# Optimization experiments

Measured on AMD Instinct MI355X. Metric: run time of the kernel, lower is better.

## Reference

```python
import jax, jax.numpy as jnp
import numpy as np

HEADS = 8
C_OUT = 256


def _gconv1x1(x, w, g):
    # x: (B, Cin, H, W); w: (Cout, Cin//g) -> grouped 1x1 conv, out (B, g, Cout//g, L)
    B, C, H, W = x.shape
    xr = x.reshape(B, g, C // g, H * W)
    wr = w.reshape(g, w.shape[0] // g, C // g)
    return jnp.einsum('god,bgdl->bgol', wr, xr)


def _sine_pe(d, L, dtype):
    # standard transformer sinusoidal PE laid out as (channels=d, positions=L)
    pos = jnp.arange(L, dtype=jnp.float32)
    i = jnp.arange(0, d, 2, dtype=jnp.float32)
    inv_freq = jnp.exp(-np.float32(np.log(10000.0)) * i / d)  # (d/2,)
    ang = inv_freq[:, None] * pos[None, :]                    # (d/2, L)
    pe = jnp.zeros((d, L), jnp.float32)
    pe = pe.at[0::2].set(jnp.sin(ang)).at[1::2].set(jnp.cos(ang))
    return pe.astype(dtype)


def setup_inputs() -> dict:
    key = jax.random.key(0)
    k1, k2, k3, k4 = jax.random.split(key, 4)
    B, Cin, H, W = 2, 256, 24, 24
    std = np.float32(np.sqrt(2.0 / C_OUT))  # kaiming_normal fan_out, relu gain
    x = jax.random.normal(k1, (B, Cin, H, W), jnp.float32)
    wq = jax.random.normal(k2, (C_OUT, Cin // HEADS), jnp.float32) * std
    wk = jax.random.normal(k3, (C_OUT, Cin // HEADS), jnp.float32) * std
    wv = jax.random.normal(k4, (C_OUT, Cin // HEADS), jnp.float32) * std
    return {"x": x, "wq": wq, "wk": wk, "wv": wv}


def reference(x, wq, wk, wv):
    B, Cin, H, W = x.shape
    g = HEADS
    d = C_OUT // g
    L = H * W
    q = _gconv1x1(x, wq, g)  # (B, g, d, L)
    k = _gconv1x1(x, wk, g)
    v = _gconv1x1(x, wv, g)
    # sinusoidal positional encoding added to keys over flattened spatial dim
    pe = _sine_pe(C_OUT, L, x.dtype)
    k = (k.reshape(B, C_OUT, L) + pe[None]).reshape(B, g, d, L)
    # NOTE: original torch code flattens batch AND heads into the attention dim
    qf = q.transpose(0, 1, 3, 2).reshape(-1, d)   # (N, d), N = B*g*L
    kf = k.transpose(2, 0, 1, 3).reshape(d, -1)   # (d, N)
    vf = v.transpose(0, 1, 3, 2).reshape(-1, d)   # (N, d)
    scale = np.float32(np.sqrt(g / C_OUT))        # = 1/sqrt(d)
    att = jax.nn.softmax(qf @ kf * scale, axis=-1)  # (N, N)
    out = att @ vf                                  # (N, d)
    out = out.reshape(B, g, L, d).transpose(0, 1, 3, 2).reshape(B, C_OUT, H, W)
    return out
```

## Files before the change

kernel.cpp:

```cpp
#include <hip/hip_runtime.h>
#include <hip/hip_bf16.h>


#define LSP   576
#define NROW  9216
#define DH    32
#define NW    8
#define KPW   (NROW / NW)
#define BN    32
#define NTILE (KPW / BN)
#define PSTR  40
#define QB    36
#define SZ    ((size_t)NROW * DH)
#define SZP   (SZ + 2048)

typedef __attribute__((ext_vector_type(8))) short bh8;
typedef __attribute__((ext_vector_type(4))) float f4;

static __device__ __forceinline__ float bf2f(unsigned short u) {
    union { unsigned int i; float f; } w; w.i = (unsigned int)u << 16; return w.f;
}
static __device__ __forceinline__ unsigned short f2bf(float x) {
    union { float f; unsigned int i; } w; w.f = x;
    unsigned int u = w.i;
    return (unsigned short)((u + 0x7fffu + ((u >> 16) & 1u)) >> 16);
}
static __device__ __forceinline__ unsigned int pkbf(float a, float b) {
    union { __hip_bfloat162 h2; unsigned int u; } w;
    w.h2 = __float22bfloat162_rn(make_float2(a, b));
    return w.u;
}

#define MFMA(a, b, c) __builtin_amdgcn_mfma_f32_16x16x32_bf16(a, b, c, 0, 0, 0)

__global__ __launch_bounds__(256) void sa_proj_kernel(
    const float* __restrict__ x,
    const float* __restrict__ wq, const float* __restrict__ wk, const float* __restrict__ wv,
    unsigned short* __restrict__ Qhi, unsigned short* __restrict__ Qlo,
    unsigned short* __restrict__ Khi, unsigned short* __restrict__ Vt)
{
    __shared__ __align__(16) float xs[32 * 40];
    __shared__ float vt[32 * 37];
    __shared__ float wqs[32 * 33], wks[32 * 33], wvs[32 * 33];
    const int t = threadIdx.x;
    const int bg = blockIdx.x >> 4;
    const int part = blockIdx.x & 15;
    const int g = bg & 7;
    const int l0 = part * 36;

    const float* xp = x + (size_t)bg * 32 * LSP + l0;
    for (int i = t; i < 32 * 9; i += 256) {
        int d = i / 9, seg = i % 9;
        *(float4*)(xs + d * 40 + seg * 4) = *(const float4*)(xp + d * LSP + seg * 4);
    }
    for (int i = t; i < 1024; i += 256) {
        int o = i >> 5, d = i & 31;
        wqs[o * 33 + d] = wq[(g * 32 + o) * 32 + d];
        wks[o * 33 + d] = wk[(g * 32 + o) * 32 + d];
        wvs[o * 33 + d] = wv[(g * 32 + o) * 32 + d];
    }
    __syncthreads();

    const float scale = 0.17677669529663687f;
    for (int idx = t; idx < 32 * 36; idx += 256) {
        const int o = idx & 31;
        const int lloc = idx >> 5;
        const int l = l0 + lloc;
        float aq = 0.f, ak = 0.f, av = 0.f;
        #pragma unroll
        for (int d = 0; d < 32; d++) {
            const float xv = xs[d * 40 + lloc];
            aq = fmaf(wqs[o * 33 + d], xv, aq);
            ak = fmaf(wks[o * 33 + d], xv, ak);
            av = fmaf(wvs[o * 33 + d], xv, av);
        }
        aq *= scale;
        const int c = g * 32 + o;
        const float i2 = (float)(c & ~1);
        const float inv = __expf(-0.035977892078031968f * i2);
        float sv, cv;
        __sincosf(inv * (float)l, &sv, &cv);
        ak += (c & 1) ? cv : sv;

        const size_t row = (size_t)bg * LSP + l;
        const unsigned short h = f2bf(aq);
        Qhi[row * 32 + o] = h;
        Qlo[row * 32 + o] = f2bf(aq - bf2f(h));
        Khi[row * 32 + o] = f2bf(ak);
        vt[o * 37 + lloc] = av;
    }
    __syncthreads();

    for (int idx = t; idx < 32 * 36; idx += 256) {
        const int d = idx / 36;
        const int cc = idx - d * 36;
        const int n = bg * LSP + l0 + cc;
        const int k = n & 31;
        const int cperm = (k < 16) ? ((k >> 2) * 8 + (k & 3))
                                   : (((k - 16) >> 2) * 8 + ((k - 16) & 3) + 4);
        Vt[(size_t)(n >> 5) * 1024 + d * 32 + cperm] = f2bf(vt[d * 37 + cc]);
    }
}

__global__ __launch_bounds__(512, 2) void sa_attn_kernel(
    const unsigned short* __restrict__ Qhi, const unsigned short* __restrict__ Qlo,
    const unsigned short* __restrict__ Khi, const unsigned short* __restrict__ Vt,
    float* __restrict__ out)
{
    __shared__ __align__(16) unsigned short shm[NW * 2 * 48 * PSTR];
    const int t = threadIdx.x;
    const int wave = t >> 6, lane = t & 63;
    const int quad = lane >> 4, l16 = lane & 15;
    const int n0 = blockIdx.x * QB;

    unsigned short* psA = shm + wave * 2 * 48 * PSTR;
    unsigned short* psB = psA + 48 * PSTR;

    const bh8 qh0 = *(const bh8*)(Qhi + (size_t)(n0 + l16) * DH + quad * 8);
    const bh8 ql0 = *(const bh8*)(Qlo + (size_t)(n0 + l16) * DH + quad * 8);
    const bh8 qh1 = *(const bh8*)(Qhi + (size_t)(n0 + 16 + l16) * DH + quad * 8);
    const bh8 ql1 = *(const bh8*)(Qlo + (size_t)(n0 + 16 + l16) * DH + quad * 8);
    const bh8 qh2 = *(const bh8*)(Qhi + (size_t)(n0 + 32 + l16) * DH + quad * 8);
    const bh8 ql2 = *(const bh8*)(Qlo + (size_t)(n0 + 32 + l16) * DH + quad * 8);

    const short oneb = (short)0x3F80;
    const bh8 ones = {oneb, oneb, oneb, oneb, oneb, oneb, oneb, oneb};

    f4 o00 = {0.f,0.f,0.f,0.f}, o01 = {0.f,0.f,0.f,0.f};
    f4 o10 = {0.f,0.f,0.f,0.f}, o11 = {0.f,0.f,0.f,0.f};
    f4 o20 = {0.f,0.f,0.f,0.f}, o21 = {0.f,0.f,0.f,0.f};
    f4 lo0 = {0.f,0.f,0.f,0.f}, lo1 = {0.f,0.f,0.f,0.f}, lo2 = {0.f,0.f,0.f,0.f};
    const f4 zf = {0.f,0.f,0.f,0.f};

    const int kbase = wave * KPW;
    const int tile0 = kbase >> 5;

    bh8 kf0 = *(const bh8*)(Khi + (size_t)(kbase + l16) * DH + quad * 8);
    bh8 kf1 = *(const bh8*)(Khi + (size_t)(kbase + 16 + l16) * DH + quad * 8);
    bh8 vf0 = *(const bh8*)(Vt + (size_t)tile0 * 1024 + l16 * 32 + quad * 8);
    bh8 vf1 = *(const bh8*)(Vt + (size_t)tile0 * 1024 + (16 + l16) * 32 + quad * 8);
    bh8 pv0 = vf0, pv1 = vf1;

    for (int tile = 0; tile < NTILE; ++tile) {
        f4 s00 = MFMA(kf0, ql0, zf); s00 = MFMA(kf0, qh0, s00);
        f4 s01 = MFMA(kf0, ql1, zf); s01 = MFMA(kf0, qh1, s01);
        f4 s02 = MFMA(kf0, ql2, zf); s02 = MFMA(kf0, qh2, s02);
        f4 s10 = MFMA(kf1, ql0, zf); s10 = MFMA(kf1, qh0, s10);
        f4 s11 = MFMA(kf1, ql1, zf); s11 = MFMA(kf1, qh1, s11);
        f4 s12 = MFMA(kf1, ql2, zf); s12 = MFMA(kf1, qh2, s12);

        const int tn = (tile + 1 < NTILE) ? tile + 1 : tile;
        const int kn = kbase + tn * BN;
        kf0 = *(const bh8*)(Khi + (size_t)(kn + l16) * DH + quad * 8);
        kf1 = *(const bh8*)(Khi + (size_t)(kn + 16 + l16) * DH + quad * 8);

        unsigned short* pc = (tile & 1) ? psB : psA;
        uint4 w0, w1, w2;
        w0.x = pkbf(__expf(s00[0]), __expf(s00[1]));
        w0.y = pkbf(__expf(s00[2]), __expf(s00[3]));
        w0.z = pkbf(__expf(s10[0]), __expf(s10[1]));
        w0.w = pkbf(__expf(s10[2]), __expf(s10[3]));
        *(uint4*)(pc + l16 * PSTR + quad * 8) = w0;
        w1.x = pkbf(__expf(s01[0]), __expf(s01[1]));
        w1.y = pkbf(__expf(s01[2]), __expf(s01[3]));
        w1.z = pkbf(__expf(s11[0]), __expf(s11[1]));
        w1.w = pkbf(__expf(s11[2]), __expf(s11[3]));
        *(uint4*)(pc + (16 + l16) * PSTR + quad * 8) = w1;
        w2.x = pkbf(__expf(s02[0]), __expf(s02[1]));
        w2.y = pkbf(__expf(s02[2]), __expf(s02[3]));
        w2.z = pkbf(__expf(s12[0]), __expf(s12[1]));
        w2.w = pkbf(__expf(s12[2]), __expf(s12[3]));
        *(uint4*)(pc + (32 + l16) * PSTR + quad * 8) = w2;

        if (tile > 0) {
            const unsigned short* pp = (tile & 1) ? psA : psB;
            const bh8 pa0 = *(const bh8*)(pp + l16 * PSTR + quad * 8);
            const bh8 pa1 = *(const bh8*)(pp + (16 + l16) * PSTR + quad * 8);
            const bh8 pa2 = *(const bh8*)(pp + (32 + l16) * PSTR + quad * 8);
            o00 = MFMA(pa0, pv0, o00); o01 = MFMA(pa0, pv1, o01);
            o10 = MFMA(pa1, pv0, o10); o11 = MFMA(pa1, pv1, o11);
            o20 = MFMA(pa2, pv0, o20); o21 = MFMA(pa2, pv1, o21);
            lo0 = MFMA(pa0, ones, lo0);
            lo1 = MFMA(pa1, ones, lo1);
            lo2 = MFMA(pa2, ones, lo2);
        }
        pv0 = vf0; pv1 = vf1;
        vf0 = *(const bh8*)(Vt + (size_t)(tile0 + tn) * 1024 + l16 * 32 + quad * 8);
        vf1 = *(const bh8*)(Vt + (size_t)(tile0 + tn) * 1024 + (16 + l16) * 32 + quad * 8);
    }
    {
        const unsigned short* pp = (NTILE & 1) ? psA : psB;
        const bh8 pa0 = *(const bh8*)(pp + l16 * PSTR + quad * 8);
        const bh8 pa1 = *(const bh8*)(pp + (16 + l16) * PSTR + quad * 8);
        const bh8 pa2 = *(const bh8*)(pp + (32 + l16) * PSTR + quad * 8);
        o00 = MFMA(pa0, pv0, o00); o01 = MFMA(pa0, pv1, o01);
        o10 = MFMA(pa1, pv0, o10); o11 = MFMA(pa1, pv1, o11);
        o20 = MFMA(pa2, pv0, o20); o21 = MFMA(pa2, pv1, o21);
        lo0 = MFMA(pa0, ones, lo0);
        lo1 = MFMA(pa1, ones, lo1);
        lo2 = MFMA(pa2, ones, lo2);
    }

    __syncthreads();
    float* mo = (float*)shm;
    float* mls = mo + NW * 1536;
    float* mp = mo + wave * 1536;
    #pragma unroll
    for (int reg = 0; reg < 4; ++reg) {
        const int q0 = quad * 4 + reg;
        mp[l16 * 48 + q0]             = o00[reg];
        mp[(16 + l16) * 48 + q0]      = o01[reg];
        mp[l16 * 48 + 16 + q0]        = o10[reg];
        mp[(16 + l16) * 48 + 16 + q0] = o11[reg];
        mp[l16 * 48 + 32 + q0]        = o20[reg];
        mp[(16 + l16) * 48 + 32 + q0] = o21[reg];
    }
    if (l16 == 0) {
        #pragma unroll
        for (int reg = 0; reg < 4; ++reg) {
            mls[wave * 48 + quad * 4 + reg]      = lo0[reg];
            mls[wave * 48 + 16 + quad * 4 + reg] = lo1[reg];
            mls[wave * 48 + 32 + quad * 4 + reg] = lo2[reg];
        }
    }
    __syncthreads();

    const int bg = n0 / LSP;
    const int l0 = n0 - bg * LSP;
    for (int c = t; c < 32 * QB; c += 512) {
        const int d = c / QB;
        const int q = c - d * QB;
        float num = 0.f, den = 0.f;
        #pragma unroll
        for (int w2 = 0; w2 < NW; ++w2) {
            num += mo[w2 * 1536 + d * 48 + q];
            den += mls[w2 * 48 + q];
        }
        out[((size_t)(bg * 32 + d)) * LSP + l0 + q] = num / den;
    }
}

extern "C" void kernel_launch(void* const* d_in, const int* in_sizes, int n_in,
                              void* d_out, int out_size, void* d_ws, size_t ws_size,
                              hipStream_t stream) {
    (void)in_sizes; (void)n_in; (void)out_size; (void)ws_size;
    const float* x  = (const float*)d_in[0];
    const float* wq = (const float*)d_in[1];
    const float* wk = (const float*)d_in[2];
    const float* wv = (const float*)d_in[3];

    unsigned short* ws = (unsigned short*)d_ws;
    unsigned short* Qhi = ws;
    unsigned short* Qlo = ws + SZP;
    unsigned short* Khi = ws + 2 * SZP;
    unsigned short* Vt  = ws + 3 * SZP;
    float* out = (float*)d_out;

    sa_proj_kernel<<<256, 256, 0, stream>>>(x, wq, wk, wv, Qhi, Qlo, Khi, Vt);
    sa_attn_kernel<<<256, 512, 0, stream>>>(Qhi, Qlo, Khi, Vt, out);
}
```

Measured before the change: 98.84 us.

## Split keys across 16 waves per block and drop P double-buffering

Doubles the waves per attention block from 8 to 16, so each wave handles half as many key tiles. It also replaces the double-buffered P tile in LDS with a single buffer that is written and then read immediately, so the P·V MFMA is no longer deferred by one tile. The cross-wave merge now runs in two phases: the first 8 waves store their partials and the second 8 add theirs into the same slots. The aim is more latency hiding and parallelism per CU, at the cost of register pressure under launch_bounds(1024,4), an extra barrier in the merge, and a serial LDS write-then-read dependency inside each tile.

After: 94.91 us. 1.04x faster.

```diff
diff --git a/kernel.cpp b/kernel.cpp
--- a/kernel.cpp
+++ b/kernel.cpp
@@ -5,14 +5,14 @@
 #define LSP   576
 #define NROW  9216
 #define DH    32
-#define NW    8
+#define NW    16
 #define KPW   (NROW / NW)
 #define BN    32
 #define NTILE (KPW / BN)
 #define PSTR  40
 #define QB    36
 #define SZ    ((size_t)NROW * DH)
-#define SZP   (SZ + 2048)
+#define SZP   (SZ + 4096)
 
 typedef __attribute__((ext_vector_type(8))) short bh8;
 typedef __attribute__((ext_vector_type(4))) float f4;
@@ -102,19 +102,18 @@
     }
 }
 
-__global__ __launch_bounds__(512, 2) void sa_attn_kernel(
+__global__ __launch_bounds__(1024, 4) void sa_attn_kernel(
     const unsigned short* __restrict__ Qhi, const unsigned short* __restrict__ Qlo,
     const unsigned short* __restrict__ Khi, const unsigned short* __restrict__ Vt,
     float* __restrict__ out)
 {
-    __shared__ __align__(16) unsigned short shm[NW * 2 * 48 * PSTR];
+    __shared__ __align__(16) unsigned short shm[NW * 48 * PSTR];
     const int t = threadIdx.x;
     const int wave = t >> 6, lane = t & 63;
     const int quad = lane >> 4, l16 = lane & 15;
     const int n0 = blockIdx.x * QB;
 
-    unsigned short* psA = shm + wave * 2 * 48 * PSTR;
-    unsigned short* psB = psA + 48 * PSTR;
+    unsigned short* psw = shm + wave * 48 * PSTR;
 
     const bh8 qh0 = *(const bh8*)(Qhi + (size_t)(n0 + l16) * DH + quad * 8);
     const bh8 ql0 = *(const bh8*)(Qlo + (size_t)(n0 + l16) * DH + quad * 8);
@@ -139,7 +138,6 @@
     bh8 kf1 = *(const bh8*)(Khi + (size_t)(kbase + 16 + l16) * DH + quad * 8);
     bh8 vf0 = *(const bh8*)(Vt + (size_t)tile0 * 1024 + l16 * 32 + quad * 8);
     bh8 vf1 = *(const bh8*)(Vt + (size_t)tile0 * 1024 + (16 + l16) * 32 + quad * 8);
-    bh8 pv0 = vf0, pv1 = vf1;
 
     for (int tile = 0; tile < NTILE; ++tile) {
         f4 s00 = MFMA(kf0, ql0, zf); s00 = MFMA(kf0, qh0, s00);
@@ -154,85 +152,93 @@
         kf0 = *(const bh8*)(Khi + (size_t)(kn + l16) * DH + quad * 8);
         kf1 = *(const bh8*)(Khi + (size_t)(kn + 16 + l16) * DH + quad * 8);
 
-        unsigned short* pc = (tile & 1) ? psB : psA;
         uint4 w0, w1, w2;
         w0.x = pkbf(__expf(s00[0]), __expf(s00[1]));
         w0.y = pkbf(__expf(s00[2]), __expf(s00[3]));
         w0.z = pkbf(__expf(s10[0]), __expf(s10[1]));
         w0.w = pkbf(__expf(s10[2]), __expf(s10[3]));
-        *(uint4*)(pc + l16 * PSTR + quad * 8) = w0;
+        *(uint4*)(psw + l16 * PSTR + quad * 8) = w0;
         w1.x = pkbf(__expf(s01[0]), __expf(s01[1]));
         w1.y = pkbf(__expf(s01[2]), __expf(s01[3]));
         w1.z = pkbf(__expf(s11[0]), __expf(s11[1]));
         w1.w = pkbf(__expf(s11[2]), __expf(s11[3]));
-        *(uint4*)(pc + (16 + l16) * PSTR + quad * 8) = w1;
+        *(uint4*)(psw + (16 + l16) * PSTR + quad * 8) = w1;
         w2.x = pkbf(__expf(s02[0]), __expf(s02[1]));
         w2.y = pkbf(__expf(s02[2]), __expf(s02[3]));
         w2.z = pkbf(__expf(s12[0]), __expf(s12[1]));
         w2.w = pkbf(__expf(s12[2]), __expf(s12[3]));
-        *(uint4*)(pc + (32 + l16) * PSTR + quad * 8) = w2;
-
-        if (tile > 0) {
-            const unsigned short* pp = (tile & 1) ? psA : psB;
-            const bh8 pa0 = *(const bh8*)(pp + l16 * PSTR + quad * 8);
-            const bh8 pa1 = *(const bh8*)(pp + (16 + l16) * PSTR + quad * 8);
-            const bh8 pa2 = *(const bh8*)(pp + (32 + l16) * PSTR + quad * 8);
-            o00 = MFMA(pa0, pv0, o00); o01 = MFMA(pa0, pv1, o01);
-            o10 = MFMA(pa1, pv0, o10); o11 = MFMA(pa1, pv1, o11);
-            o20 = MFMA(pa2, pv0, o20); o21 = MFMA(pa2, pv1, o21);
-            lo0 = MFMA(pa0, ones, lo0);
-            lo1 = MFMA(pa1, ones, lo1);
-            lo2 = MFMA(pa2, ones, lo2);
-        }
-        pv0 = vf0; pv1 = vf1;
-        vf0 = *(const bh8*)(Vt + (size_t)(tile0 + tn) * 1024 + l16 * 32 + quad * 8);
-        vf1 = *(const bh8*)(Vt + (size_t)(tile0 + tn) * 1024 + (16 + l16) * 32 + quad * 8);
-    }
-    {
-        const unsigned short* pp = (NTILE & 1) ? psA : psB;
-        const bh8 pa0 = *(const bh8*)(pp + l16 * PSTR + quad * 8);
-        const bh8 pa1 = *(const bh8*)(pp + (16 + l16) * PSTR + quad * 8);
-        const bh8 pa2 = *(const bh8*)(pp + (32 + l16) * PSTR + quad * 8);
-        o00 = MFMA(pa0, pv0, o00); o01 = MFMA(pa0, pv1, o01);
-        o10 = MFMA(pa1, pv0, o10); o11 = MFMA(pa1, pv1, o11);
-        o20 = MFMA(pa2, pv0, o20); o21 = MFMA(pa2, pv1, o21);
+        *(uint4*)(psw + (32 + l16) * PSTR + quad * 8) = w2;
+
+        const bh8 pa0 = *(const bh8*)(psw + l16 * PSTR + quad * 8);
+        const bh8 pa1 = *(const bh8*)(psw + (16 + l16) * PSTR + quad * 8);
+        const bh8 pa2 = *(const bh8*)(psw + (32 + l16) * PSTR + quad * 8);
+        o00 = MFMA(pa0, vf0, o00); o01 = MFMA(pa0, vf1, o01);
+        o10 = MFMA(pa1, vf0, o10); o11 = MFMA(pa1, vf1, o11);
+        o20 = MFMA(pa2, vf0, o20); o21 = MFMA(pa2, vf1, o21);
         lo0 = MFMA(pa0, ones, lo0);
         lo1 = MFMA(pa1, ones, lo1);
         lo2 = MFMA(pa2, ones, lo2);
+
+        vf0 = *(const bh8*)(Vt + (size_t)(tile0 + tn) * 1024 + l16 * 32 + quad * 8);
+        vf1 = *(const bh8*)(Vt + (size_t)(tile0 + tn) * 1024 + (16 + l16) * 32 + quad * 8);
     }
 
     __syncthreads();
     float* mo = (float*)shm;
-    float* mls = mo + NW * 1536;
-    float* mp = mo + wave * 1536;
-    #pragma unroll
-    for (int reg = 0; reg < 4; ++reg) {
-        const int q0 = quad * 4 + reg;
-        mp[l16 * 48 + q0]             = o00[reg];
-        mp[(16 + l16) * 48 + q0]      = o01[reg];
-        mp[l16 * 48 + 16 + q0]        = o10[reg];
-        mp[(16 + l16) * 48 + 16 + q0] = o11[reg];
-        mp[l16 * 48 + 32 + q0]        = o20[reg];
-        mp[(16 + l16) * 48 + 32 + q0] = o21[reg];
-    }
-    if (l16 == 0) {
+    float* mls = mo + 8 * 1536;
+    const int mw = wave & 7;
+    float* mp = mo + mw * 1536;
+    if (wave < 8) {
         #pragma unroll
         for (int reg = 0; reg < 4; ++reg) {
-            mls[wave * 48 + quad * 4 + reg]      = lo0[reg];
-            mls[wave * 48 + 16 + quad * 4 + reg] = lo1[reg];
-            mls[wave * 48 + 32 + quad * 4 + reg] = lo2[reg];
+            const int q0 = quad * 4 + reg;
+            mp[l16 * 48 + q0]             = o00[reg];
+            mp[(16 + l16) * 48 + q0]      = o01[reg];
+            mp[l16 * 48 + 16 + q0]        = o10[reg];
+            mp[(16 + l16) * 48 + 16 + q0] = o11[reg];
+            mp[l16 * 48 + 32 + q0]        = o20[reg];
+            mp[(16 + l16) * 48 + 32 + q0] = o21[reg];
+        }
+        if (l16 == 0) {
+            #pragma unroll
+            for (int reg = 0; reg < 4; ++reg) {
+                mls[mw * 48 + quad * 4 + reg]      = lo0[reg];
+                mls[mw * 48 + 16 + quad * 4 + reg] = lo1[reg];
+                mls[mw * 48 + 32 + quad * 4 + reg] = lo2[reg];
+            }
+        }
+    }
+    __syncthreads();
+    if (wave >= 8) {
+        #pragma unroll
+        for (int reg = 0; reg < 4; ++reg) {
+            const int q0 = quad * 4 + reg;
+            mp[l16 * 48 + q0]             += o00[reg];
+            mp[(16 + l16) * 48 + q0]      += o01[reg];
+            mp[l16 * 48 + 16 + q0]        += o10[reg];
+            mp[(16 + l16) * 48 + 16 + q0] += o11[reg];
+            mp[l16 * 48 + 32 + q0]        += o20[reg];
+            mp[(16 + l16) * 48 + 32 + q0] += o21[reg];
+        }
+        if (l16 == 0) {
+            #pragma unroll
+            for (int reg = 0; reg < 4; ++reg) {
+                mls[mw * 48 + quad * 4 + reg]      += lo0[reg];
+                mls[mw * 48 + 16 + quad * 4 + reg] += lo1[reg];
+                mls[mw * 48 + 32 + quad * 4 + reg] += lo2[reg];
+            }
         }
     }
     __syncthreads();
 
     const int bg = n0 / LSP;
     const int l0 = n0 - bg * LSP;
-    for (int c = t; c < 32 * QB; c += 512) {
+    for (int c = t; c < 32 * QB; c += 1024) {
         const int d = c / QB;
         const int q = c - d * QB;
         float num = 0.f, den = 0.f;
         #pragma unroll
-        for (int w2 = 0; w2 < NW; ++w2) {
+        for (int w2 = 0; w2 < 8; ++w2) {
             num += mo[w2 * 1536 + d * 48 + q];
             den += mls[w2 * 48 + q];
         }
@@ -257,5 +263,5 @@
     float* out = (float*)d_out;
 
     sa_proj_kernel<<<256, 256, 0, stream>>>(x, wq, wk, wv, Qhi, Qlo, Khi, Vt);
-    sa_attn_kernel<<<256, 512, 0, stream>>>(Qhi, Qlo, Khi, Vt, out);
-}
+    sa_attn_kernel<<<256, 1024, 0, stream>>>(Qhi, Qlo, Khi, Vt, out);
+}
```
